# Optimization experiments

Hardware: AMD Instinct MI355X
Metric: run time of the kernel (lower is better)

The kernel has to match this reference:

```python
import jax, jax.numpy as jnp
import numpy as np
from jax import lax

TH = 1.0  # fire threshold (init kwarg th)


def setup_inputs() -> dict:
    key = jax.random.key(0)
    k0, k1, k2 = jax.random.split(key, 3)
    B, T, C = 32, 3000, 512
    hs_pad = jax.random.normal(k0, (B, T, C), dtype=jnp.float32)
    hs_mask = jnp.ones((B, 1, T), dtype=jnp.int32)  # espnet-style [B,1,T] mask, 1=valid
    # Conv1d(C, C, k=5) weight layout [out, in, k], fan-in scaled
    conv_w = jax.random.normal(k1, (C, C, 5), dtype=jnp.float32) * (1.0 / np.sqrt(C * 5))
    conv_b = jnp.zeros((C,), dtype=jnp.float32)
    # Linear(C, 1): stored transposed as [C, 1]
    lin_w = jax.random.normal(k2, (C, 1), dtype=jnp.float32) * (1.0 / np.sqrt(C))
    lin_b = jnp.zeros((1,), dtype=jnp.float32)
    return dict(hs_pad=hs_pad, hs_mask=hs_mask, conv_w=conv_w, conv_b=conv_b,
                lin_w=lin_w, lin_b=lin_b)


def _cif_single(alpha, h, th):
    """Integrate-and-fire for one sequence. alpha:[T], h:[T,C] -> [T,C] (zero padded)."""
    T, C = h.shape

    def step(carry, inp):
        acc, hacc = carry
        a, hu = inp
        acc2 = acc + a
        fired = acc2 >= th
        a1 = th - acc  # = th - (acc2 - a)
        emit = jnp.where(fired, hacc + a1 * hu, jnp.zeros_like(hu))
        new_acc = jnp.where(fired, a - a1, acc2)
        new_h = jnp.where(fired, (a - a1) * hu, hacc + a * hu)
        return (new_acc, new_h), (fired, emit)

    (acc_f, h_f), (fired, emits) = lax.scan(
        step, (jnp.float32(0.0), jnp.zeros((C,), h.dtype)), (alpha, h))
    nfire = jnp.cumsum(fired.astype(jnp.int32))
    idx = jnp.where(fired, nfire - 1, T)  # non-fired steps dump into scratch row T
    out = jnp.zeros((T + 1, C), h.dtype).at[idx].add(emits)
    # tail emission: remaining mass >= th/2
    tail = acc_f >= th * 0.5
    tail_idx = jnp.where(tail, nfire[-1], T)
    out = out.at[tail_idx].add(jnp.where(tail, h_f, jnp.zeros_like(h_f)))
    return out[:T]  # fires <= T always (alpha < 1 = th)


def _forward(hs_pad, hs_mask, conv_w, conv_b, lin_w, lin_b):
    B, T, C = hs_pad.shape
    # Conv1d(C,C,5,pad=2) on [B,C,T]  (note: self.norm is never used in the torch forward)
    x = lax.conv_general_dilated(hs_pad.transpose(0, 2, 1), conv_w, (1,), [(2, 2)],
                                 dimension_numbers=('NCH', 'OIH', 'NCH'))
    x = jax.nn.relu(x + conv_b[None, :, None])  # [B,C,T]
    alpha = jax.nn.sigmoid(jnp.einsum('bct,co->bto', x, lin_w) + lin_b)  # [B,T,1]
    # ys_pad=None -> T_y = 0; loss computed BEFORE masking (as in torch)
    loss_pen = jnp.abs(alpha.sum(axis=1) - 0.0).sum()
    a = alpha[..., 0] * (hs_mask[:, 0, :] != 0).astype(alpha.dtype)  # masked_fill(mask==0, 0)
    cs = jax.vmap(lambda av, hv: _cif_single(av, hv, TH))(a, hs_pad)  # [B,T,C]
    cs_mask = jnp.any(cs != 0.0, axis=-1)[:, None, :]  # [B,1,T]
    return cs, cs_mask, loss_pen


def reference(hs_pad, hs_mask, conv_w, conv_b, lin_w, lin_b):
    return _forward(hs_pad, hs_mask, conv_w, conv_b, lin_w, lin_b)
```

## Files before the change

### kernel.cpp

```cpp
#include <hip/hip_runtime.h>
#include <math.h>

#define B_ 32
#define T_ 3000
#define C_ 512
#define THf 1.0f
#define KW 2560

typedef _Float16 f16;
typedef _Float16 half8 __attribute__((ext_vector_type(8)));
typedef _Float16 half4 __attribute__((ext_vector_type(4)));
typedef float floatx4 __attribute__((ext_vector_type(4)));

#define WHI_OFF   0
#define WLO_OFF   2621440
#define PL_OFF    5242880
#define ALPHA_OFF 8314880
#define SEGI_OFF  8698880
#define SEGW_OFF  9466880
#define TOT_OFF   10234880

#define CS_SIZE  ((size_t)B_ * T_ * C_)
#define MASK_OFF CS_SIZE
#define LOSS_OFF (CS_SIZE + (size_t)B_ * T_)

__global__ __launch_bounds__(256) void w_prep_kernel(
    const float* __restrict__ W, f16* __restrict__ whi, f16* __restrict__ wlo)
{
    int idx = blockIdx.x * 256 + threadIdx.x;
    if (idx >= 512 * KW) return;
    int o = idx / KW;
    int c = idx - o * KW;
    int k = c >> 9, i = c & 511;
    float w = W[o * KW + i * 5 + k];
    f16 h = (f16)w;
    f16 l = (f16)((w - (float)h) * 2048.0f);
    whi[idx] = h;
    wlo[idx] = l;
}

#define LDA 72
#define LDW 40
#define A_ROWS 132

__global__ __launch_bounds__(256, 2) void conv_alpha_mfma(
    const float* __restrict__ hs, const f16* __restrict__ whi_g,
    const f16* __restrict__ wlo_g, const float* __restrict__ conv_b,
    const float* __restrict__ lin_w, float* __restrict__ pl)
{
    __shared__ f16 sm[2 * A_ROWS * LDA + 2 * 128 * LDW];
    f16* Ahi = sm;
    f16* Alo = sm + A_ROWS * LDA;
    f16* Whi = sm + 2 * A_ROWS * LDA;
    f16* Wlo = Whi + 128 * LDW;

    int tid = threadIdx.x;
    int bid = blockIdx.x;
    int nb  = bid & 3;
    int mtg = bid >> 2;
    int b   = mtg / 24;
    int mt  = mtg - b * 24;
    int t0  = mt * 128;

    int wid = tid >> 6, l = tid & 63;
    int wm = wid >> 1, wn = wid & 1;
    int l15 = l & 15, l4 = l >> 4;

    const float* hb = hs + (size_t)b * T_ * C_;
    int o0 = nb * 128;

    floatx4 acc1[4][4], acc2[4][4];
#pragma unroll
    for (int mf = 0; mf < 4; ++mf)
#pragma unroll
        for (int nf = 0; nf < 4; ++nf) {
            acc1[mf][nf] = (floatx4)0.f;
            acc2[mf][nf] = (floatx4)0.f;
        }

    for (int ic = 0; ic < 8; ++ic) {
        int i0 = ic * 64;
        __syncthreads();
        for (int j = tid; j < A_ROWS * 16; j += 256) {
            int r = j >> 4, c4 = j & 15;
            int t = t0 - 2 + r;
            float4 v = make_float4(0.f, 0.f, 0.f, 0.f);
            if (t >= 0 && t < T_)
                v = *(const float4*)(hb + (size_t)t * C_ + i0 + c4 * 4);
            f16 h0 = (f16)v.x, h1 = (f16)v.y, h2 = (f16)v.z, h3 = (f16)v.w;
            half4 hh = {h0, h1, h2, h3};
            half4 ll = {(f16)((v.x - (float)h0) * 2048.f),
                        (f16)((v.y - (float)h1) * 2048.f),
                        (f16)((v.z - (float)h2) * 2048.f),
                        (f16)((v.w - (float)h3) * 2048.f)};
            int off = r * LDA + c4 * 4;
            *(half4*)(Ahi + off) = hh;
            *(half4*)(Alo + off) = ll;
        }
        for (int k = 0; k < 5; ++k) {
            for (int sub = 0; sub < 2; ++sub) {
                __syncthreads();
                int i32 = i0 + sub * 32;
                for (int j = tid; j < 512; j += 256) {
                    int r = j >> 2, cg = j & 3;
                    size_t gidx = (size_t)(o0 + r) * KW + k * 512 + i32 + cg * 8;
                    half8 wh = *(const half8*)(whi_g + gidx);
                    half8 wl = *(const half8*)(wlo_g + gidx);
                    int off = r * LDW + cg * 8;
                    *(half8*)(Whi + off) = wh;
                    *(half8*)(Wlo + off) = wl;
                }
                __syncthreads();
                half8 ah[4], al[4], bh[4], bl[4];
#pragma unroll
                for (int f = 0; f < 4; ++f) {
                    int ar = wm * 64 + f * 16 + l15 + k;
                    int aoff = ar * LDA + sub * 32 + l4 * 8;
                    ah[f] = *(const half8*)(Ahi + aoff);
                    al[f] = *(const half8*)(Alo + aoff);
                    int wr = wn * 64 + f * 16 + l15;
                    int woff = wr * LDW + l4 * 8;
                    bh[f] = *(const half8*)(Whi + woff);
                    bl[f] = *(const half8*)(Wlo + woff);
                }
#pragma unroll
                for (int mf = 0; mf < 4; ++mf)
#pragma unroll
                    for (int nf = 0; nf < 4; ++nf) {
                        acc1[mf][nf] = __builtin_amdgcn_mfma_f32_16x16x32_f16(
                            ah[mf], bh[nf], acc1[mf][nf], 0, 0, 0);
                        acc2[mf][nf] = __builtin_amdgcn_mfma_f32_16x16x32_f16(
                            al[mf], bh[nf], acc2[mf][nf], 0, 0, 0);
                        acc2[mf][nf] = __builtin_amdgcn_mfma_f32_16x16x32_f16(
                            ah[mf], bl[nf], acc2[mf][nf], 0, 0, 0);
                    }
            }
        }
    }

    float cb[4], lw[4];
#pragma unroll
    for (int nf = 0; nf < 4; ++nf) {
        int o = o0 + wn * 64 + nf * 16 + l15;
        cb[nf] = conv_b[o];
        lw[nf] = lin_w[o];
    }
    float* plb = pl + (size_t)(nb * 2 + wn) * (B_ * T_) + b * T_;
#pragma unroll
    for (int mf = 0; mf < 4; ++mf) {
#pragma unroll
        for (int reg = 0; reg < 4; ++reg) {
            float v = 0.f;
#pragma unroll
            for (int nf = 0; nf < 4; ++nf) {
                float c = acc1[mf][nf][reg] + acc2[mf][nf][reg] * (1.0f / 2048.0f);
                v += fmaxf(c + cb[nf], 0.f) * lw[nf];
            }
            v += __shfl_xor(v, 1);
            v += __shfl_xor(v, 2);
            v += __shfl_xor(v, 4);
            v += __shfl_xor(v, 8);
            int trow = t0 + wm * 64 + mf * 16 + l4 * 4 + reg;
            if (l15 == reg && trow < T_) plb[trow] = v;
        }
    }
}

__global__ __launch_bounds__(256) void alpha_combine_kernel(
    const float* __restrict__ pl, const float* __restrict__ lin_b,
    float* __restrict__ alpha)
{
    int idx = blockIdx.x * 256 + threadIdx.x;
    if (idx >= B_ * T_) return;
    float s = lin_b[0];
#pragma unroll
    for (int p = 0; p < 8; ++p) s += pl[(size_t)p * (B_ * T_) + idx];
    alpha[idx] = 1.f / (1.f + expf(-s));
}

__global__ __launch_bounds__(64) void scan_kernel(
    float* __restrict__ alpha, const int* __restrict__ mask,
    int2* __restrict__ seg_i, float2* __restrict__ seg_w,
    int* __restrict__ total_rows, float* __restrict__ out_loss)
{
    int lane = threadIdx.x;
    float lsum = 0.f;
    if (lane < B_) {
        const float4* ap = (const float4*)(alpha + lane * T_);
        const int4*   mp = (const int4*)(mask + lane * T_);
        float* astore = alpha + lane * T_;
        int2*   si = seg_i + lane * T_;
        float2* sw = seg_w + lane * T_;

        float acc = 0.f, leftover = 0.f;
        int nf = 0, prev_t = -1;

        float4 c0 = ap[0], c1 = ap[1];
        int4   m0 = mp[0], m1 = mp[1];
        for (int tc = 0; tc < T_ / 8; ++tc) {
            float4 n0, n1; int4 nm0, nm1;
            if (tc + 1 < T_ / 8) {
                n0 = ap[(tc + 1) * 2]; n1 = ap[(tc + 1) * 2 + 1];
                nm0 = mp[(tc + 1) * 2]; nm1 = mp[(tc + 1) * 2 + 1];
            }
            float av[8] = {c0.x, c0.y, c0.z, c0.w, c1.x, c1.y, c1.z, c1.w};
            int   mv[8] = {m0.x, m0.y, m0.z, m0.w, m1.x, m1.y, m1.z, m1.w};
#pragma unroll
            for (int u = 0; u < 8; ++u) {
                int t = tc * 8 + u;
                float araw = av[u];
                lsum += araw;
                float a = (mv[u] != 0) ? araw : 0.f;
                astore[t] = a;
                float acc2 = acc + a;
                float a1 = THf - acc;
                if (acc2 >= THf) {
                    si[nf] = make_int2(prev_t, t);
                    sw[nf] = make_float2(leftover, a1);
                    float rem = a - a1;
                    leftover = rem;
                    acc = rem;
                    prev_t = t;
                    ++nf;
                } else {
                    acc = acc2;
                }
            }
            c0 = n0; c1 = n1; m0 = nm0; m1 = nm1;
        }
        int tot = nf;
        if (acc >= 0.5f * THf) {
            si[nf] = make_int2(prev_t, T_);
            sw[nf] = make_float2(leftover, 0.f);
            ++tot;
        }
        total_rows[lane] = tot;
        lsum = fabsf(lsum);
    }
#pragma unroll
    for (int off = 16; off >= 1; off >>= 1) lsum += __shfl_down(lsum, off);
    if (lane == 0) out_loss[0] = lsum;
}

__global__ __launch_bounds__(128) void emit_kernel(
    const float* __restrict__ hs, const float* __restrict__ alpha,
    const int2* __restrict__ seg_i, const float2* __restrict__ seg_w,
    const int* __restrict__ total_rows, float* __restrict__ out)
{
    int blk = blockIdx.x;
    int b = blk / T_;
    int r = blk % T_;
    int tid = threadIdx.x;

    float4* cs4 = (float4*)(out + ((size_t)b * T_ + r) * C_);
    float* maskp = out + MASK_OFF + (size_t)b * T_ + r;
    int tot = total_rows[b];

    if (r >= tot) {
        float4 z; z.x = 0.f; z.y = 0.f; z.z = 0.f; z.w = 0.f;
        cs4[tid] = z;
        if (tid == 0) *maskp = 0.f;
        return;
    }
    int2   si = seg_i[b * T_ + r];
    float2 sw = seg_w[b * T_ + r];
    const float4* hb = (const float4*)(hs + (size_t)b * T_ * C_);
    const float*  ab = alpha + b * T_;

    float4 acc; acc.x = 0.f; acc.y = 0.f; acc.z = 0.f; acc.w = 0.f;
    int ts = si.x, te = si.y;
    if (ts >= 0) {
        float4 h = hb[(size_t)ts * (C_ / 4) + tid];
        acc.x = sw.x * h.x; acc.y = sw.x * h.y; acc.z = sw.x * h.z; acc.w = sw.x * h.w;
    }
    for (int t = ts + 1; t < te; ++t) {
        float a = ab[t];
        float4 h = hb[(size_t)t * (C_ / 4) + tid];
        acc.x = fmaf(a, h.x, acc.x); acc.y = fmaf(a, h.y, acc.y);
        acc.z = fmaf(a, h.z, acc.z); acc.w = fmaf(a, h.w, acc.w);
    }
    if (te < T_) {
        float4 h = hb[(size_t)te * (C_ / 4) + tid];
        acc.x = fmaf(sw.y, h.x, acc.x); acc.y = fmaf(sw.y, h.y, acc.y);
        acc.z = fmaf(sw.y, h.z, acc.z); acc.w = fmaf(sw.y, h.w, acc.w);
    }
    cs4[tid] = acc;
    if (tid == 0) *maskp = 1.f;
}

extern "C" void kernel_launch(void* const* d_in, const int* in_sizes, int n_in,
                              void* d_out, int out_size, void* d_ws, size_t ws_size,
                              hipStream_t stream)
{
    const float* hs     = (const float*)d_in[0];
    const int*   hmask  = (const int*)d_in[1];
    const float* conv_w = (const float*)d_in[2];
    const float* conv_b = (const float*)d_in[3];
    const float* lin_w  = (const float*)d_in[4];
    const float* lin_b  = (const float*)d_in[5];
    float* out = (float*)d_out;
    char*  ws  = (char*)d_ws;

    f16*    whi   = (f16*)(ws + WHI_OFF);
    f16*    wlo   = (f16*)(ws + WLO_OFF);
    float*  pl    = (float*)(ws + PL_OFF);
    float*  alpha = (float*)(ws + ALPHA_OFF);
    int2*   seg_i = (int2*)(ws + SEGI_OFF);
    float2* seg_w = (float2*)(ws + SEGW_OFF);
    int*    tot   = (int*)(ws + TOT_OFF);

    w_prep_kernel<<<(512 * KW + 255) / 256, 256, 0, stream>>>(conv_w, whi, wlo);
    conv_alpha_mfma<<<B_ * 24 * 4, 256, 0, stream>>>(hs, whi, wlo, conv_b, lin_w, pl);
    alpha_combine_kernel<<<(B_ * T_ + 255) / 256, 256, 0, stream>>>(pl, lin_b, alpha);
    scan_kernel<<<1, 64, 0, stream>>>(alpha, hmask, seg_i, seg_w, tot, out + LOSS_OFF);
    emit_kernel<<<B_ * T_, 128, 0, stream>>>(hs, alpha, seg_i, seg_w, tot, out);
}
```

Measured before the change: 1.132 ms.

## Double-buffer conv weights via async global-to-LDS loads with swizzled A tile

Repacks the split fp16 weights into a k-major, 8-element-interleaved layout so each weight sub-tile can be copied straight from global memory into LDS with global_load_lds. The next sub-tile is loaded into a second buffer while the current one feeds the MFMAs, which cuts the per-step sync count from two to one. The activation tile drops its row padding in favour of an XOR swizzle to avoid bank conflicts, and the MFMA block is wrapped in raised wave priority. The costs are more LDS for double buffering and reliance on the direct-to-LDS load path's visibility rules, since no explicit vmcnt wait precedes the barrier.

```diff
diff --git a/kernel.cpp b/kernel.cpp
--- a/kernel.cpp
+++ b/kernel.cpp
@@ -9,8 +9,10 @@
 
 typedef _Float16 f16;
 typedef _Float16 half8 __attribute__((ext_vector_type(8)));
-typedef _Float16 half4 __attribute__((ext_vector_type(4)));
 typedef float floatx4 __attribute__((ext_vector_type(4)));
+
+#define GLOBAL_AS __attribute__((address_space(1)))
+#define LDS_AS __attribute__((address_space(3)))
 
 #define WHI_OFF   0
 #define WLO_OFF   2621440
@@ -29,30 +31,31 @@
 {
     int idx = blockIdx.x * 256 + threadIdx.x;
     if (idx >= 512 * KW) return;
-    int o = idx / KW;
-    int c = idx - o * KW;
-    int k = c >> 9, i = c & 511;
+    int ie = idx & 7;
+    int o  = (idx >> 3) & 511;
+    int i8 = (idx >> 12) & 63;
+    int k  = idx >> 18;
+    int i  = i8 * 8 + ie;
     float w = W[o * KW + i * 5 + k];
     f16 h = (f16)w;
-    f16 l = (f16)((w - (float)h) * 2048.0f);
     whi[idx] = h;
-    wlo[idx] = l;
-}
-
-#define LDA 72
-#define LDW 40
+    wlo[idx] = (f16)((w - (float)h) * 2048.0f);
+}
+
 #define A_ROWS 132
+#define ALO_OFF_E  8448
+#define WB_OFF_E   16896
+#define WB_ARR_E   4096
 
 __global__ __launch_bounds__(256, 2) void conv_alpha_mfma(
     const float* __restrict__ hs, const f16* __restrict__ whi_g,
     const f16* __restrict__ wlo_g, const float* __restrict__ conv_b,
     const float* __restrict__ lin_w, float* __restrict__ pl)
 {
-    __shared__ f16 sm[2 * A_ROWS * LDA + 2 * 128 * LDW];
+    __shared__ f16 sm[33280];
     f16* Ahi = sm;
-    f16* Alo = sm + A_ROWS * LDA;
-    f16* Whi = sm + 2 * A_ROWS * LDA;
-    f16* Wlo = Whi + 128 * LDW;
+    f16* Alo = sm + ALO_OFF_E;
+    f16* Wb  = sm + WB_OFF_E;
 
     int tid = threadIdx.x;
     int bid = blockIdx.x;
@@ -78,64 +81,83 @@
             acc2[mf][nf] = (floatx4)0.f;
         }
 
-    for (int ic = 0; ic < 8; ++ic) {
-        int i0 = ic * 64;
+    auto issue_w = [&](int s2) {
+        int buf = s2 & 1;
+        int ic2 = s2 / 10, kk2 = s2 % 10;
+        int k2 = kk2 >> 1, sub2 = kk2 & 1;
+        int i8b = ic2 * 8 + sub2 * 4;
+#pragma unroll
+        for (int rr = 0; rr < 4; ++rr) {
+            int r = wid * 4 + rr;
+            int arr = r >> 3, kc = (r >> 1) & 3, oh = r & 1;
+            const f16* gsrc = (arr ? wlo_g : whi_g) +
+                ((size_t)((k2 * 64 + i8b + kc) * 512 + o0 + oh * 64 + l)) * 8;
+            f16* ldst = Wb + (buf * 2 + arr) * WB_ARR_E + (kc * 128 + oh * 64) * 8;
+            __builtin_amdgcn_global_load_lds((const GLOBAL_AS void*)gsrc,
+                                             (LDS_AS void*)ldst, 16, 0, 0);
+        }
+    };
+
+    issue_w(0);
+
+    for (int s = 0; s < 80; ++s) {
+        int ic = s / 10, kk = s % 10;
+        int k = kk >> 1, sub = kk & 1;
+        int buf = s & 1;
+
+        if (kk == 0) {
+            int i0 = ic * 64;
+            for (int j = tid; j < A_ROWS * 8; j += 256) {
+                int r = j >> 3, c = j & 7;
+                int t = t0 - 2 + r;
+                float4 v0 = make_float4(0.f, 0.f, 0.f, 0.f);
+                float4 v1 = v0;
+                if ((unsigned)t < (unsigned)T_) {
+                    const float4* p = (const float4*)(hb + (size_t)t * C_ + i0 + c * 8);
+                    v0 = p[0]; v1 = p[1];
+                }
+                float vv[8] = {v0.x, v0.y, v0.z, v0.w, v1.x, v1.y, v1.z, v1.w};
+                half8 hh, ll;
+#pragma unroll
+                for (int q = 0; q < 8; ++q) {
+                    f16 x = (f16)vv[q];
+                    hh[q] = x;
+                    ll[q] = (f16)((vv[q] - (float)x) * 2048.f);
+                }
+                int off = r * 64 + (c ^ (r & 7)) * 8;
+                *(half8*)(Ahi + off) = hh;
+                *(half8*)(Alo + off) = ll;
+            }
+            __syncthreads();
+        }
+
+        if (s + 1 < 80) issue_w(s + 1);
+
+        half8 ah[4], al[4], bh[4], bl[4];
+#pragma unroll
+        for (int f = 0; f < 4; ++f) {
+            int ar = wm * 64 + f * 16 + l15 + k;
+            int aoff = ar * 64 + ((((sub << 2) | l4) ^ (ar & 7)) << 3);
+            ah[f] = *(const half8*)(Ahi + aoff);
+            al[f] = *(const half8*)(Alo + aoff);
+            int wrow = l4 * 128 + wn * 64 + f * 16 + l15;
+            bh[f] = *(const half8*)(Wb + (buf * 2 + 0) * WB_ARR_E + wrow * 8);
+            bl[f] = *(const half8*)(Wb + (buf * 2 + 1) * WB_ARR_E + wrow * 8);
+        }
+        __builtin_amdgcn_s_setprio(1);
+#pragma unroll
+        for (int mf = 0; mf < 4; ++mf)
+#pragma unroll
+            for (int nf = 0; nf < 4; ++nf) {
+                acc1[mf][nf] = __builtin_amdgcn_mfma_f32_16x16x32_f16(
+                    ah[mf], bh[nf], acc1[mf][nf], 0, 0, 0);
+                acc2[mf][nf] = __builtin_amdgcn_mfma_f32_16x16x32_f16(
+                    al[mf], bh[nf], acc2[mf][nf], 0, 0, 0);
+                acc2[mf][nf] = __builtin_amdgcn_mfma_f32_16x16x32_f16(
+                    ah[mf], bl[nf], acc2[mf][nf], 0, 0, 0);
+            }
+        __builtin_amdgcn_s_setprio(0);
         __syncthreads();
-        for (int j = tid; j < A_ROWS * 16; j += 256) {
-            int r = j >> 4, c4 = j & 15;
-            int t = t0 - 2 + r;
-            float4 v = make_float4(0.f, 0.f, 0.f, 0.f);
-            if (t >= 0 && t < T_)
-                v = *(const float4*)(hb + (size_t)t * C_ + i0 + c4 * 4);
-            f16 h0 = (f16)v.x, h1 = (f16)v.y, h2 = (f16)v.z, h3 = (f16)v.w;
-            half4 hh = {h0, h1, h2, h3};
-            half4 ll = {(f16)((v.x - (float)h0) * 2048.f),
-                        (f16)((v.y - (float)h1) * 2048.f),
-                        (f16)((v.z - (float)h2) * 2048.f),
-                        (f16)((v.w - (float)h3) * 2048.f)};
-            int off = r * LDA + c4 * 4;
-            *(half4*)(Ahi + off) = hh;
-            *(half4*)(Alo + off) = ll;
-        }
-        for (int k = 0; k < 5; ++k) {
-            for (int sub = 0; sub < 2; ++sub) {
-                __syncthreads();
-                int i32 = i0 + sub * 32;
-                for (int j = tid; j < 512; j += 256) {
-                    int r = j >> 2, cg = j & 3;
-                    size_t gidx = (size_t)(o0 + r) * KW + k * 512 + i32 + cg * 8;
-                    half8 wh = *(const half8*)(whi_g + gidx);
-                    half8 wl = *(const half8*)(wlo_g + gidx);
-                    int off = r * LDW + cg * 8;
-                    *(half8*)(Whi + off) = wh;
-                    *(half8*)(Wlo + off) = wl;
-                }
-                __syncthreads();
-                half8 ah[4], al[4], bh[4], bl[4];
-#pragma unroll
-                for (int f = 0; f < 4; ++f) {
-                    int ar = wm * 64 + f * 16 + l15 + k;
-                    int aoff = ar * LDA + sub * 32 + l4 * 8;
-                    ah[f] = *(const half8*)(Ahi + aoff);
-                    al[f] = *(const half8*)(Alo + aoff);
-                    int wr = wn * 64 + f * 16 + l15;
-                    int woff = wr * LDW + l4 * 8;
-                    bh[f] = *(const half8*)(Whi + woff);
-                    bl[f] = *(const half8*)(Wlo + woff);
-                }
-#pragma unroll
-                for (int mf = 0; mf < 4; ++mf)
-#pragma unroll
-                    for (int nf = 0; nf < 4; ++nf) {
-                        acc1[mf][nf] = __builtin_amdgcn_mfma_f32_16x16x32_f16(
-                            ah[mf], bh[nf], acc1[mf][nf], 0, 0, 0);
-                        acc2[mf][nf] = __builtin_amdgcn_mfma_f32_16x16x32_f16(
-                            al[mf], bh[nf], acc2[mf][nf], 0, 0, 0);
-                        acc2[mf][nf] = __builtin_amdgcn_mfma_f32_16x16x32_f16(
-                            ah[mf], bl[nf], acc2[mf][nf], 0, 0, 0);
-                    }
-            }
-        }
     }
 
     float cb[4], lw[4];
```

After: 971.3 us. 1.17x faster.
